# Performance work log

Hardware: AMD Instinct MI355X
Metric: run time of the kernel (lower is better)

Reference implementation:

```python
import jax, jax.numpy as jnp
import numpy as np
import math

B, S, D, H = 4, 2048, 1024, 16
DK = D // H  # 64


def setup_inputs() -> dict:
    key = jax.random.key(0)
    ks = jax.random.split(key, 8)
    sc = 1.0 / math.sqrt(D)
    Q = jax.random.normal(ks[0], (B, S, D), dtype=jnp.float32)
    K = jax.random.normal(ks[1], (B, S, D), dtype=jnp.float32)
    V = jax.random.normal(ks[2], (B, S, D), dtype=jnp.float32)
    # per-head projection weights, stacked: [H, D, DK]
    Wq = jax.random.normal(ks[3], (H, D, DK), dtype=jnp.float32) * sc
    Wk = jax.random.normal(ks[4], (H, D, DK), dtype=jnp.float32) * sc
    Wv = jax.random.normal(ks[5], (H, D, DK), dtype=jnp.float32) * sc
    Wo = jax.random.normal(ks[6], (D, D), dtype=jnp.float32) * sc
    bo = jax.random.normal(ks[7], (D,), dtype=jnp.float32) * sc
    mask = jnp.tril(jnp.ones((S, S), dtype=bool))  # causal
    return {"Q": Q, "K": K, "V": V, "mask": mask,
            "Wq": Wq, "Wk": Wk, "Wv": Wv, "Wo": Wo, "bo": bo}


def reference(Q, K, V, mask, Wq, Wk, Wv, Wo, bo):
    # batched per-head projections: [B,S,D] x [H,D,DK] -> [B,H,S,DK]
    q = jnp.einsum('bsd,hdk->bhsk', Q, Wq)
    k = jnp.einsum('bsd,hdk->bhsk', K, Wk)
    v = jnp.einsum('bsd,hdk->bhsk', V, Wv)
    # NOTE: source scales by k.shape[-1]/sqrt(d_k) = d_k/sqrt(d_k) = sqrt(d_k)
    scale = jnp.float32(DK / math.sqrt(DK))
    w = jnp.einsum('bhsk,bhtk->bhst', q, k) * scale  # [B,H,S,S]
    w = jnp.where(mask[None, None, :, :], w, jnp.float32(-jnp.inf))
    w = jax.nn.softmax(w, axis=-1)
    out = jnp.einsum('bhst,bhtk->bhsk', w, v)  # [B,H,S,DK]
    # concat heads along last dim (head order preserved): [B,S,D]
    concat = out.transpose(0, 2, 1, 3).reshape(B, S, D)
    # output projection (dropout p=0 -> identity in eval)
    return concat @ Wo.T + bo
```

## Files before the change

### kernel.cpp

```cpp
#include <hip/hip_runtime.h>
#include <math.h>


#define BB 4
#define SS 2048
#define DD 1024
#define HH 16
#define DKK 64
#define MM (BB * SS)

typedef unsigned short u16;
typedef _Float16 f16x8 __attribute__((ext_vector_type(8)));
typedef float f32x4 __attribute__((ext_vector_type(4)));
typedef __attribute__((address_space(1))) unsigned int gas_u32;
typedef __attribute__((address_space(3))) unsigned int las_u32;

__device__ __forceinline__ float bf2f(u16 u) {
    union { unsigned int i; float f; } c;
    c.i = ((unsigned int)u) << 16;
    return c.f;
}
__device__ __forceinline__ u16 f2h(float f) {
    _Float16 h = (_Float16)f;
    return __builtin_bit_cast(u16, h);
}
__device__ __forceinline__ void split1(float x, u16& hi, u16& lo) {
    _Float16 hh = (_Float16)x;
    hi = __builtin_bit_cast(u16, hh);
    lo = f2h(x - (float)hh);
}
__device__ __forceinline__ void gld16(const void* g, void* l) {
    __builtin_amdgcn_global_load_lds((gas_u32*)g, (las_u32*)l, 16, 0, 0);
}

__global__ void sniff_kernel(const u16* t0, const u16* t1, const u16* t2,
                             const u16* t3, const u16* t4, const u16* t5,
                             const u16* t6, const u16* t7, int* flags)
{
    const u16* ptrs[8] = {t0, t1, t2, t3, t4, t5, t6, t7};
    const u16* p = ptrs[blockIdx.x];
    int tid = threadIdx.x;
    int cnt = 0;
    #pragma unroll
    for (int i = 0; i < 8; i++) {
        u16 v = p[tid * 8 + i];
        int e = (v >> 7) & 0xFF;
        if (e >= 0xF0 || (e <= 0x0F && (v & 0x7FFF) != 0)) cnt++;
    }
    #pragma unroll
    for (int off = 32; off; off >>= 1) cnt += __shfl_down(cnt, off);
    if (tid == 0) flags[blockIdx.x] = (cnt >= 4) ? 1 : 0;
}

__global__ __launch_bounds__(256) void split_x_kernel(
    const void* __restrict__ X, const int* __restrict__ flags, int fidx,
    u16* __restrict__ Xh, u16* __restrict__ Xl)
{
    const int xf = flags[fidx];
    size_t idx = ((size_t)blockIdx.x * 256 + threadIdx.x) * 8;
    float x[8];
    if (xf) {
        float4 a = *(const float4*)((const float*)X + idx);
        float4 b = *(const float4*)((const float*)X + idx + 4);
        x[0] = a.x; x[1] = a.y; x[2] = a.z; x[3] = a.w;
        x[4] = b.x; x[5] = b.y; x[6] = b.z; x[7] = b.w;
    } else {
        ushort4 a = *(const ushort4*)((const u16*)X + idx);
        ushort4 b = *(const ushort4*)((const u16*)X + idx + 4);
        x[0] = bf2f(a.x); x[1] = bf2f(a.y); x[2] = bf2f(a.z); x[3] = bf2f(a.w);
        x[4] = bf2f(b.x); x[5] = bf2f(b.y); x[6] = bf2f(b.z); x[7] = bf2f(b.w);
    }
    union { u16 u[8]; uint4 v; } H, L;
    #pragma unroll
    for (int i = 0; i < 8; i++) split1(x[i], H.u[i], L.u[i]);
    *(uint4*)(Xh + idx) = H.v;
    *(uint4*)(Xl + idx) = L.v;
}

__global__ __launch_bounds__(256) void split_wqkv_kernel(
    const void* __restrict__ Wq, const void* __restrict__ Wk, const void* __restrict__ Wv,
    const int* __restrict__ flags, u16* __restrict__ Wth, u16* __restrict__ Wtl)
{
    const int z = blockIdx.z, h = blockIdx.y, kc = blockIdx.x;
    const void* __restrict__ W = (z == 0) ? Wq : (z == 1) ? Wk : Wv;
    const int wf = flags[3 + z];
    __shared__ float T[64][65];
    const int t = threadIdx.x;
    {
        const int kk = t >> 2, ns = (t & 3) * 16;
        const size_t base = (size_t)h * DD * DKK + (size_t)(kc * 64 + kk) * DKK + ns;
        #pragma unroll
        for (int j = 0; j < 4; j++) {
            if (wf) {
                float4 v = *(const float4*)((const float*)W + base + 4 * j);
                T[kk][ns + 4 * j + 0] = v.x; T[kk][ns + 4 * j + 1] = v.y;
                T[kk][ns + 4 * j + 2] = v.z; T[kk][ns + 4 * j + 3] = v.w;
            } else {
                ushort4 v = *(const ushort4*)((const u16*)W + base + 4 * j);
                T[kk][ns + 4 * j + 0] = bf2f(v.x); T[kk][ns + 4 * j + 1] = bf2f(v.y);
                T[kk][ns + 4 * j + 2] = bf2f(v.z); T[kk][ns + 4 * j + 3] = bf2f(v.w);
            }
        }
    }
    __syncthreads();
    {
        const int n = t >> 2, ks = (t & 3) * 16;
        union { u16 u[16]; uint4 v[2]; } Hv, Lv;
        #pragma unroll
        for (int i = 0; i < 16; i++) split1(T[ks + i][n], Hv.u[i], Lv.u[i]);
        size_t ob = ((size_t)(z * HH + h) * DKK + n) * DD + kc * 64 + ks;
        *(uint4*)(Wth + ob)     = Hv.v[0];
        *(uint4*)(Wth + ob + 8) = Hv.v[1];
        *(uint4*)(Wtl + ob)     = Lv.v[0];
        *(uint4*)(Wtl + ob + 8) = Lv.v[1];
    }
}

__global__ __launch_bounds__(256, 4) void proj_v3_kernel(
    const u16* __restrict__ Xh, const u16* __restrict__ Xl,
    const u16* __restrict__ Wth, const u16* __restrict__ Wtl,
    u16* __restrict__ out, int z)
{
    const int h0 = blockIdx.y * 2;
    const int m0 = blockIdx.x * 128;

    __shared__ __align__(16) u16 WH[128 * 64];
    __shared__ __align__(16) u16 WL[128 * 64];

    const int tid  = threadIdx.x;
    const int lane = tid & 63, wave = tid >> 6;
    const int quad = lane >> 4, ln = lane & 15;

    const int lr = lane >> 3, lg = (lane & 7) ^ (lane >> 3);
    const size_t wsrc0 = ((size_t)((z * HH + h0) * DKK) + wave * 32 + lr) * DD + lg * 8;
    const size_t arow = (size_t)(m0 + wave * 32 + ln) * DD + quad * 8;

    f32x4 acc[2][8];
    #pragma unroll
    for (int mh = 0; mh < 2; mh++)
        #pragma unroll
        for (int nt = 0; nt < 8; nt++)
            acc[mh][nt] = (f32x4){0.f, 0.f, 0.f, 0.f};

    for (int kbase = 0; kbase < DD; kbase += 64) {
        __syncthreads();
        f16x8 a_h[2][2], a_l[2][2];
        #pragma unroll
        for (int kh = 0; kh < 2; kh++)
            #pragma unroll
            for (int mh = 0; mh < 2; mh++) {
                size_t o = arow + (size_t)(mh * 16) * DD + kbase + kh * 32;
                a_h[kh][mh] = __builtin_bit_cast(f16x8, *(const uint4*)(Xh + o));
                a_l[kh][mh] = __builtin_bit_cast(f16x8, *(const uint4*)(Xl + o));
            }
        #pragma unroll
        for (int j = 0; j < 4; j++) {
            gld16(Wth + wsrc0 + (size_t)j * 8 * DD + kbase, &WH[(wave * 32 + j * 8) * 64]);
            gld16(Wtl + wsrc0 + (size_t)j * 8 * DD + kbase, &WL[(wave * 32 + j * 8) * 64]);
        }
        asm volatile("s_waitcnt vmcnt(0)" ::: "memory");
        __syncthreads();

        #pragma unroll
        for (int kh = 0; kh < 2; kh++) {
            const int kg = ((kh * 4 + quad) ^ (ln & 7)) * 8;
            #pragma unroll
            for (int nt = 0; nt < 8; nt++) {
                const int n = nt * 16 + ln;
                f16x8 bh = __builtin_bit_cast(f16x8, *(const uint4*)&WH[n * 64 + kg]);
                f16x8 bl = __builtin_bit_cast(f16x8, *(const uint4*)&WL[n * 64 + kg]);
                #pragma unroll
                for (int mh = 0; mh < 2; mh++) {
                    acc[mh][nt] = __builtin_amdgcn_mfma_f32_16x16x32_f16(a_l[kh][mh], bh, acc[mh][nt], 0, 0, 0);
                    acc[mh][nt] = __builtin_amdgcn_mfma_f32_16x16x32_f16(a_h[kh][mh], bl, acc[mh][nt], 0, 0, 0);
                    acc[mh][nt] = __builtin_amdgcn_mfma_f32_16x16x32_f16(a_h[kh][mh], bh, acc[mh][nt], 0, 0, 0);
                }
            }
        }
    }

    #pragma unroll
    for (int mh = 0; mh < 2; mh++)
        #pragma unroll
        for (int r = 0; r < 4; r++) {
            int m = m0 + wave * 32 + mh * 16 + quad * 4 + r;
            int b = m >> 11, s = m & 2047;
            #pragma unroll
            for (int nt = 0; nt < 8; nt++) {
                int head = h0 + (nt >> 2);
                u16* op = out + (((size_t)(b * HH + head) * SS + s)) * DKK;
                op[(nt & 3) * 16 + ln] = f2h(acc[mh][nt][r]);
            }
        }
}

__global__ __launch_bounds__(512) void attn_kernel(
    const u16* __restrict__ qb, const u16* __restrict__ kb,
    const u16* __restrict__ vb, u16* __restrict__ cath, u16* __restrict__ catl)
{
    __shared__ __align__(16) u16 Kt[64 * 72];
    __shared__ __align__(16) u16 Vt[64 * 72];
    __shared__ __align__(16) u16 Pw[8][16 * 72];

    const int tid  = threadIdx.x;
    const int lane = tid & 63, wave = tid >> 6;
    const int quad = lane >> 4, ln = lane & 15;

    const int p  = blockIdx.x;
    const int bh = (p >> 6) * 8 + (p & 7);
    const int pairidx = (p >> 3) & 7;
    const int b = bh >> 4, h = bh & 15;

    const int skey = tid >> 3, sseg = (tid & 7) * 8;
    const int vkey = tid & 63, vdkb = (tid >> 6) * 8;

    const u16* kbp = kb + (size_t)bh * SS * DKK;
    const u16* vbp = vb + (size_t)bh * SS * DKK;

    #pragma unroll 1
    for (int half = 0; half < 2; half++) {
        const int xt = half == 0 ? 15 - pairidx : pairidx;
        const int qbase = xt * 128;
        const int ktmax = 2 * xt + 1;

        const int wq = qbase + wave * 16;
        const int diagkt = wq >> 6;
        const int wqmax = wq + 15;

        const u16* qp = qb + ((size_t)bh * SS + wq + ln) * DKK;
        f16x8 qf0 = __builtin_bit_cast(f16x8, *(const uint4*)(qp + quad * 8));
        f16x8 qf1 = __builtin_bit_cast(f16x8, *(const uint4*)(qp + 32 + quad * 8));

        f32x4 acc[4];
        #pragma unroll
        for (int n = 0; n < 4; n++) acc[n] = (f32x4){0.f, 0.f, 0.f, 0.f};
        float mrow[4], lrow[4];
        #pragma unroll
        for (int r = 0; r < 4; r++) { mrow[r] = -INFINITY; lrow[r] = 0.f; }

        {
            uint4 ka = *(const uint4*)(kbp + (size_t)skey * DKK + sseg);
            uint4 va = *(const uint4*)(vbp + (size_t)vkey * DKK + vdkb);
            *(uint4*)&Kt[skey * 72 + sseg] = ka;
            u16 vv[8];
            *(uint4*)&vv[0] = va;
            #pragma unroll
            for (int i = 0; i < 8; i++)
                Vt[(vdkb + i) * 72 + vkey] = vv[i];
        }
        __syncthreads();

        for (int kt = 0; kt <= ktmax; ++kt) {
            uint4 ka, va;
            const bool pfb = (kt < ktmax);
            if (pfb) {
                ka = *(const uint4*)(kbp + (size_t)((kt + 1) * 64 + skey) * DKK + sseg);
                va = *(const uint4*)(vbp + (size_t)((kt + 1) * 64 + vkey) * DKK + vdkb);
            }

            if (kt * 64 <= wqmax) {
                f32x4 sa[4];
                #pragma unroll
                for (int n = 0; n < 4; n++) {
                    sa[n] = (f32x4){0.f, 0.f, 0.f, 0.f};
                    f16x8 kf0 = __builtin_bit_cast(f16x8,
                        *(const uint4*)&Kt[(n * 16 + ln) * 72 + quad * 8]);
                    sa[n] = __builtin_amdgcn_mfma_f32_16x16x32_f16(qf0, kf0, sa[n], 0, 0, 0);
                    f16x8 kf1 = __builtin_bit_cast(f16x8,
                        *(const uint4*)&Kt[(n * 16 + ln) * 72 + 32 + quad * 8]);
                    sa[n] = __builtin_amdgcn_mfma_f32_16x16x32_f16(qf1, kf1, sa[n], 0, 0, 0);
                }

                float sc[4][4];
                const bool diag = (kt == diagkt);
                #pragma unroll
                for (int n = 0; n < 4; n++)
                    #pragma unroll
                    for (int r = 0; r < 4; r++) {
                        float s = sa[n][r] * 8.0f;
                        if (diag && (kt * 64 + n * 16 + ln) > (wq + quad * 4 + r))
                            s = -INFINITY;
                        sc[n][r] = s;
                    }

                float rmax[4];
                #pragma unroll
                for (int r = 0; r < 4; r++)
                    rmax[r] = fmaxf(fmaxf(sc[0][r], sc[1][r]), fmaxf(sc[2][r], sc[3][r]));
                #pragma unroll
                for (int off = 1; off < 16; off <<= 1)
                    #pragma unroll
                    for (int r = 0; r < 4; r++)
                        rmax[r] = fmaxf(rmax[r], __shfl_xor(rmax[r], off));
                float alpha[4];
                #pragma unroll
                for (int r = 0; r < 4; r++) {
                    float mn = fmaxf(mrow[r], rmax[r]);
                    alpha[r] = __expf(mrow[r] - mn);
                    mrow[r] = mn;
                }
                u16* pw = Pw[wave];
                float lsum[4] = {0.f, 0.f, 0.f, 0.f};
                #pragma unroll
                for (int n = 0; n < 4; n++)
                    #pragma unroll
                    for (int r = 0; r < 4; r++) {
                        float pp = __expf(sc[n][r] - mrow[r]);
                        _Float16 ph = (_Float16)pp;
                        pw[(quad * 4 + r) * 72 + n * 16 + ln] = __builtin_bit_cast(u16, ph);
                        lsum[r] += (float)ph;
                    }
                #pragma unroll
                for (int off = 1; off < 16; off <<= 1)
                    #pragma unroll
                    for (int r = 0; r < 4; r++)
                        lsum[r] += __shfl_xor(lsum[r], off);
                #pragma unroll
                for (int r = 0; r < 4; r++)
                    lrow[r] = lrow[r] * alpha[r] + lsum[r];
                #pragma unroll
                for (int n = 0; n < 4; n++)
                    #pragma unroll
                    for (int r = 0; r < 4; r++)
                        acc[n][r] *= alpha[r];

                asm volatile("s_waitcnt lgkmcnt(0)" ::: "memory");
                f16x8 pf0 = __builtin_bit_cast(f16x8, *(const uint4*)&pw[ln * 72 + quad * 8]);
                f16x8 pf1 = __builtin_bit_cast(f16x8, *(const uint4*)&pw[ln * 72 + 32 + quad * 8]);

                #pragma unroll
                for (int n = 0; n < 4; n++) {
                    f16x8 vf0 = __builtin_bit_cast(f16x8,
                        *(const uint4*)&Vt[(n * 16 + ln) * 72 + quad * 8]);
                    acc[n] = __builtin_amdgcn_mfma_f32_16x16x32_f16(pf0, vf0, acc[n], 0, 0, 0);
                    f16x8 vf1 = __builtin_bit_cast(f16x8,
                        *(const uint4*)&Vt[(n * 16 + ln) * 72 + 32 + quad * 8]);
                    acc[n] = __builtin_amdgcn_mfma_f32_16x16x32_f16(pf1, vf1, acc[n], 0, 0, 0);
                }
            }

            __syncthreads();
            if (pfb) {
                *(uint4*)&Kt[skey * 72 + sseg] = ka;
                u16 vv[8];
                *(uint4*)&vv[0] = va;
                #pragma unroll
                for (int i = 0; i < 8; i++)
                    Vt[(vdkb + i) * 72 + vkey] = vv[i];
            }
            __syncthreads();
        }

        #pragma unroll
        for (int r = 0; r < 4; r++) {
            float inv = 1.0f / lrow[r];
            int row = wq + quad * 4 + r;
            size_t o = ((size_t)b * SS + row) * DD + h * DKK;
            #pragma unroll
            for (int n = 0; n < 4; n++) {
                float v = acc[n][r] * inv;
                u16 hh, ll;
                split1(v, hh, ll);
                cath[o + n * 16 + ln] = hh;
                catl[o + n * 16 + ln] = ll;
            }
        }
    }
}

__global__ __launch_bounds__(256, 4) void outproj_v3_kernel(
    const u16* __restrict__ Ah, const u16* __restrict__ Al,
    const u16* __restrict__ Woh, const u16* __restrict__ Wol,
    const void* __restrict__ bo, const int* __restrict__ flags,
    float* __restrict__ out)
{
    const int n0 = blockIdx.y * 128;
    const int m0 = blockIdx.x * 128;

    __shared__ __align__(16) u16 WH[128 * 64];
    __shared__ __align__(16) u16 WL[128 * 64];

    const int tid  = threadIdx.x;
    const int lane = tid & 63, wave = tid >> 6;
    const int quad = lane >> 4, ln = lane & 15;

    const int lr = lane >> 3, lg = (lane & 7) ^ (lane >> 3);
    const size_t wsrc0 = ((size_t)(n0 + wave * 32 + lr)) * DD + lg * 8;
    const size_t arow  = (size_t)(m0 + wave * 32 + ln) * DD + quad * 8;

    f32x4 acc[2][8];
    #pragma unroll
    for (int mh = 0; mh < 2; mh++)
        #pragma unroll
        for (int nt = 0; nt < 8; nt++)
            acc[mh][nt] = (f32x4){0.f, 0.f, 0.f, 0.f};

    for (int kbase = 0; kbase < DD; kbase += 64) {
        __syncthreads();
        f16x8 a_h[2][2], a_l[2][2];
        #pragma unroll
        for (int kh = 0; kh < 2; kh++)
            #pragma unroll
            for (int mh = 0; mh < 2; mh++) {
                size_t o = arow + (size_t)(mh * 16) * DD + kbase + kh * 32;
                a_h[kh][mh] = __builtin_bit_cast(f16x8, *(const uint4*)(Ah + o));
                a_l[kh][mh] = __builtin_bit_cast(f16x8, *(const uint4*)(Al + o));
            }
        #pragma unroll
        for (int j = 0; j < 4; j++) {
            gld16(Woh + wsrc0 + (size_t)j * 8 * DD + kbase, &WH[(wave * 32 + j * 8) * 64]);
            gld16(Wol + wsrc0 + (size_t)j * 8 * DD + kbase, &WL[(wave * 32 + j * 8) * 64]);
        }
        asm volatile("s_waitcnt vmcnt(0)" ::: "memory");
        __syncthreads();

        #pragma unroll
        for (int kh = 0; kh < 2; kh++) {
            const int kg = ((kh * 4 + quad) ^ (ln & 7)) * 8;
            #pragma unroll
            for (int nt = 0; nt < 8; nt++) {
                const int n = nt * 16 + ln;
                f16x8 bh = __builtin_bit_cast(f16x8, *(const uint4*)&WH[n * 64 + kg]);
                f16x8 bl = __builtin_bit_cast(f16x8, *(const uint4*)&WL[n * 64 + kg]);
                #pragma unroll
                for (int mh = 0; mh < 2; mh++) {
                    acc[mh][nt] = __builtin_amdgcn_mfma_f32_16x16x32_f16(a_l[kh][mh], bh, acc[mh][nt], 0, 0, 0);
                    acc[mh][nt] = __builtin_amdgcn_mfma_f32_16x16x32_f16(a_h[kh][mh], bl, acc[mh][nt], 0, 0, 0);
                    acc[mh][nt] = __builtin_amdgcn_mfma_f32_16x16x32_f16(a_h[kh][mh], bh, acc[mh][nt], 0, 0, 0);
                }
            }
        }
    }

    const int bf = flags[7];
    float bias[8];
    #pragma unroll
    for (int nt = 0; nt < 8; nt++) {
        int n = n0 + nt * 16 + ln;
        bias[nt] = bf ? ((const float*)bo)[n] : bf2f(((const u16*)bo)[n]);
    }
    #pragma unroll
    for (int mh = 0; mh < 2; mh++)
        #pragma unroll
        for (int r = 0; r < 4; r++) {
            int m = m0 + wave * 32 + mh * 16 + quad * 4 + r;
            float* op = out + (size_t)m * DD + n0;
            #pragma unroll
            for (int nt = 0; nt < 8; nt++)
                op[nt * 16 + ln] = acc[mh][nt][r] + bias[nt];
        }
}

extern "C" void kernel_launch(void* const* d_in, const int* in_sizes, int n_in,
                              void* d_out, int out_size, void* d_ws, size_t ws_size,
                              hipStream_t stream)
{
    const void* Q = d_in[0];
    const void* K = d_in[1];
    const void* V = d_in[2];
    const int widx = (n_in >= 9) ? 4 : 3;
    const void* Wq = d_in[widx + 0];
    const void* Wk = d_in[widx + 1];
    const void* Wv = d_in[widx + 2];
    const void* Wo = d_in[widx + 3];
    const void* bo = d_in[widx + 4];
    float* out = (float*)d_out;

    const size_t per = (size_t)BB * HH * SS * DKK;
    u16* qb = (u16*)d_ws;
    u16* kb = qb + per;
    u16* vb = kb + per;
    u16* xc = vb + per;
    u16* Xh = xc;
    u16* Xl = xc + per;
    u16* cath = xc;
    u16* catl = xc + per;
    const size_t wtn = (size_t)3 * HH * DKK * DD;
    u16* Wth = xc + 2 * per;
    u16* Wtl = Wth + wtn;
    u16* Woh = Wtl + wtn;
    u16* Wol = Woh + (size_t)DD * DD;
    int* flags = (int*)(Wol + (size_t)DD * DD);

    sniff_kernel<<<8, 64, 0, stream>>>(
        (const u16*)Q, (const u16*)K, (const u16*)V,
        (const u16*)Wq, (const u16*)Wk, (const u16*)Wv,
        (const u16*)Wo, (const u16*)bo, flags);

    split_wqkv_kernel<<<dim3(DD / 64, HH, 3), 256, 0, stream>>>(
        Wq, Wk, Wv, flags, Wth, Wtl);
    split_x_kernel<<<(DD * DD) / 2048, 256, 0, stream>>>(Wo, flags, 6, Woh, Wol);

    dim3 gp(MM / 128, HH / 2);
    split_x_kernel<<<(MM * DD) / 2048, 256, 0, stream>>>(Q, flags, 0, Xh, Xl);
    proj_v3_kernel<<<gp, 256, 0, stream>>>(Xh, Xl, Wth, Wtl, qb, 0);
    split_x_kernel<<<(MM * DD) / 2048, 256, 0, stream>>>(K, flags, 1, Xh, Xl);
    proj_v3_kernel<<<gp, 256, 0, stream>>>(Xh, Xl, Wth, Wtl, kb, 1);
    split_x_kernel<<<(MM * DD) / 2048, 256, 0, stream>>>(V, flags, 2, Xh, Xl);
    proj_v3_kernel<<<gp, 256, 0, stream>>>(Xh, Xl, Wth, Wtl, vb, 2);

    attn_kernel<<<(SS / 256) * BB * HH, 512, 0, stream>>>(qb, kb, vb, cath, catl);

    outproj_v3_kernel<<<dim3(MM / 128, DD / 128), 256, 0, stream>>>(
        cath, catl, Woh, Wol, bo, flags, out);
}
```

Baseline: 490.0 us.

## Fuse input split into QKV projection and double-buffer swizzled attention tiles

Removes the three split_x passes by reading the raw Q/K/V inputs directly inside the projection kernel and splitting them into high/low f16 on the fly. The three projection launches merge into one grid indexed by blockIdx.z. The attention kernel switches from padded LDS tiles to XOR-swizzled 64-wide tiles, double-buffers K/V, and drops one barrier per key tile. The cost is extra conversion ALU work on the A operand, repeated once per head-pair block instead of once per input. It also raises attention LDS use, which may lower occupancy.

Measured after the change: 470.6 us. 1.04x faster.

```diff
diff --git a/kernel.cpp b/kernel.cpp
--- a/kernel.cpp
+++ b/kernel.cpp
@@ -116,11 +116,16 @@
     }
 }
 
-__global__ __launch_bounds__(256, 4) void proj_v3_kernel(
-    const u16* __restrict__ Xh, const u16* __restrict__ Xl,
+__global__ __launch_bounds__(256, 4) void proj_v4_kernel(
+    const void* __restrict__ Q, const void* __restrict__ K, const void* __restrict__ V,
     const u16* __restrict__ Wth, const u16* __restrict__ Wtl,
-    u16* __restrict__ out, int z)
-{
+    const int* __restrict__ flags,
+    u16* __restrict__ qb, u16* __restrict__ kb, u16* __restrict__ vb)
+{
+    const int z = blockIdx.z;
+    const void* __restrict__ X = (z == 0) ? Q : (z == 1) ? K : V;
+    u16* __restrict__ out      = (z == 0) ? qb : (z == 1) ? kb : vb;
+    const int xf = flags[z];
     const int h0 = blockIdx.y * 2;
     const int m0 = blockIdx.x * 128;
 
@@ -150,8 +155,23 @@
             #pragma unroll
             for (int mh = 0; mh < 2; mh++) {
                 size_t o = arow + (size_t)(mh * 16) * DD + kbase + kh * 32;
-                a_h[kh][mh] = __builtin_bit_cast(f16x8, *(const uint4*)(Xh + o));
-                a_l[kh][mh] = __builtin_bit_cast(f16x8, *(const uint4*)(Xl + o));
+                float x[8];
+                if (xf) {
+                    float4 a = *(const float4*)((const float*)X + o);
+                    float4 b = *(const float4*)((const float*)X + o + 4);
+                    x[0] = a.x; x[1] = a.y; x[2] = a.z; x[3] = a.w;
+                    x[4] = b.x; x[5] = b.y; x[6] = b.z; x[7] = b.w;
+                } else {
+                    ushort4 a = *(const ushort4*)((const u16*)X + o);
+                    ushort4 b = *(const ushort4*)((const u16*)X + o + 4);
+                    x[0] = bf2f(a.x); x[1] = bf2f(a.y); x[2] = bf2f(a.z); x[3] = bf2f(a.w);
+                    x[4] = bf2f(b.x); x[5] = bf2f(b.y); x[6] = bf2f(b.z); x[7] = bf2f(b.w);
+                }
+                union { u16 u[8]; f16x8 v; } H, L;
+                #pragma unroll
+                for (int i = 0; i < 8; i++) split1(x[i], H.u[i], L.u[i]);
+                a_h[kh][mh] = H.v;
+                a_l[kh][mh] = L.v;
             }
         #pragma unroll
         for (int j = 0; j < 4; j++) {
@@ -198,9 +218,9 @@
     const u16* __restrict__ qb, const u16* __restrict__ kb,
     const u16* __restrict__ vb, u16* __restrict__ cath, u16* __restrict__ catl)
 {
-    __shared__ __align__(16) u16 Kt[64 * 72];
-    __shared__ __align__(16) u16 Vt[64 * 72];
-    __shared__ __align__(16) u16 Pw[8][16 * 72];
+    __shared__ __align__(16) u16 Kt[2][64 * 64];
+    __shared__ __align__(16) u16 Vt[2][64 * 64];
+    __shared__ __align__(16) u16 Pw[8][16 * 64];
 
     const int tid  = threadIdx.x;
     const int lane = tid & 63, wave = tid >> 6;
@@ -211,7 +231,8 @@
     const int pairidx = (p >> 3) & 7;
     const int b = bh >> 4, h = bh & 15;
 
-    const int skey = tid >> 3, sseg = (tid & 7) * 8;
+    const int skey = tid >> 3, kgrp = tid & 7;
+    const int koff = skey * 64 + ((kgrp ^ (skey & 7)) << 3);
     const int vkey = tid & 63, vdkb = (tid >> 6) * 8;
 
     const u16* kbp = kb + (size_t)bh * SS * DKK;
@@ -239,35 +260,41 @@
         for (int r = 0; r < 4; r++) { mrow[r] = -INFINITY; lrow[r] = 0.f; }
 
         {
-            uint4 ka = *(const uint4*)(kbp + (size_t)skey * DKK + sseg);
+            uint4 ka = *(const uint4*)(kbp + (size_t)skey * DKK + kgrp * 8);
             uint4 va = *(const uint4*)(vbp + (size_t)vkey * DKK + vdkb);
-            *(uint4*)&Kt[skey * 72 + sseg] = ka;
+            *(uint4*)&Kt[0][koff] = ka;
             u16 vv[8];
             *(uint4*)&vv[0] = va;
             #pragma unroll
-            for (int i = 0; i < 8; i++)
-                Vt[(vdkb + i) * 72 + vkey] = vv[i];
+            for (int i = 0; i < 8; i++) {
+                int row = vdkb + i;
+                Vt[0][row * 64 + (((vkey >> 3) ^ (row & 7)) << 3) + (vkey & 7)] = vv[i];
+            }
         }
         __syncthreads();
 
+        int cur = 0;
         for (int kt = 0; kt <= ktmax; ++kt) {
             uint4 ka, va;
             const bool pfb = (kt < ktmax);
             if (pfb) {
-                ka = *(const uint4*)(kbp + (size_t)((kt + 1) * 64 + skey) * DKK + sseg);
+                ka = *(const uint4*)(kbp + (size_t)((kt + 1) * 64 + skey) * DKK + kgrp * 8);
                 va = *(const uint4*)(vbp + (size_t)((kt + 1) * 64 + vkey) * DKK + vdkb);
             }
 
             if (kt * 64 <= wqmax) {
+                const u16* KT = Kt[cur];
+                const u16* VT = Vt[cur];
                 f32x4 sa[4];
                 #pragma unroll
                 for (int n = 0; n < 4; n++) {
                     sa[n] = (f32x4){0.f, 0.f, 0.f, 0.f};
+                    const int krow = n * 16 + ln;
                     f16x8 kf0 = __builtin_bit_cast(f16x8,
-                        *(const uint4*)&Kt[(n * 16 + ln) * 72 + quad * 8]);
+                        *(const uint4*)&KT[krow * 64 + ((quad ^ (ln & 7)) << 3)]);
                     sa[n] = __builtin_amdgcn_mfma_f32_16x16x32_f16(qf0, kf0, sa[n], 0, 0, 0);
                     f16x8 kf1 = __builtin_bit_cast(f16x8,
-                        *(const uint4*)&Kt[(n * 16 + ln) * 72 + 32 + quad * 8]);
+                        *(const uint4*)&KT[krow * 64 + (((quad + 4) ^ (ln & 7)) << 3)]);
                     sa[n] = __builtin_amdgcn_mfma_f32_16x16x32_f16(qf1, kf1, sa[n], 0, 0, 0);
                 }
 
@@ -307,7 +334,9 @@
                     for (int r = 0; r < 4; r++) {
                         float pp = __expf(sc[n][r] - mrow[r]);
                         _Float16 ph = (_Float16)pp;
-                        pw[(quad * 4 + r) * 72 + n * 16 + ln] = __builtin_bit_cast(u16, ph);
+                        const int row = quad * 4 + r;
+                        pw[row * 64 + (((n * 2 + (ln >> 3)) ^ (row & 7)) << 3) + (ln & 7)]
+                            = __builtin_bit_cast(u16, ph);
                         lsum[r] += (float)ph;
                     }
                 #pragma unroll
@@ -325,30 +354,35 @@
                         acc[n][r] *= alpha[r];
 
                 asm volatile("s_waitcnt lgkmcnt(0)" ::: "memory");
-                f16x8 pf0 = __builtin_bit_cast(f16x8, *(const uint4*)&pw[ln * 72 + quad * 8]);
-                f16x8 pf1 = __builtin_bit_cast(f16x8, *(const uint4*)&pw[ln * 72 + 32 + quad * 8]);
+                f16x8 pf0 = __builtin_bit_cast(f16x8,
+                    *(const uint4*)&pw[ln * 64 + ((quad ^ (ln & 7)) << 3)]);
+                f16x8 pf1 = __builtin_bit_cast(f16x8,
+                    *(const uint4*)&pw[ln * 64 + (((quad + 4) ^ (ln & 7)) << 3)]);
 
                 #pragma unroll
                 for (int n = 0; n < 4; n++) {
+                    const int vrow = n * 16 + ln;
                     f16x8 vf0 = __builtin_bit_cast(f16x8,
-                        *(const uint4*)&Vt[(n * 16 + ln) * 72 + quad * 8]);
+                        *(const uint4*)&VT[vrow * 64 + ((quad ^ (ln & 7)) << 3)]);
                     acc[n] = __builtin_amdgcn_mfma_f32_16x16x32_f16(pf0, vf0, acc[n], 0, 0, 0);
                     f16x8 vf1 = __builtin_bit_cast(f16x8,
-                        *(const uint4*)&Vt[(n * 16 + ln) * 72 + 32 + quad * 8]);
+                        *(const uint4*)&VT[vrow * 64 + (((quad + 4) ^ (ln & 7)) << 3)]);
                     acc[n] = __builtin_amdgcn_mfma_f32_16x16x32_f16(pf1, vf1, acc[n], 0, 0, 0);
                 }
             }
 
-            __syncthreads();
             if (pfb) {
-                *(uint4*)&Kt[skey * 72 + sseg] = ka;
+                *(uint4*)&Kt[cur ^ 1][koff] = ka;
                 u16 vv[8];
                 *(uint4*)&vv[0] = va;
                 #pragma unroll
-                for (int i = 0; i < 8; i++)
-                    Vt[(vdkb + i) * 72 + vkey] = vv[i];
+                for (int i = 0; i < 8; i++) {
+                    int row = vdkb + i;
+                    Vt[cur ^ 1][row * 64 + (((vkey >> 3) ^ (row & 7)) << 3) + (vkey & 7)] = vv[i];
+                }
             }
             __syncthreads();
+            cur ^= 1;
         }
 
         #pragma unroll
@@ -470,13 +504,10 @@
     u16* qb = (u16*)d_ws;
     u16* kb = qb + per;
     u16* vb = kb + per;
-    u16* xc = vb + per;
-    u16* Xh = xc;
-    u16* Xl = xc + per;
-    u16* cath = xc;
-    u16* catl = xc + per;
+    u16* cath = vb + per;
+    u16* catl = cath + per;
     const size_t wtn = (size_t)3 * HH * DKK * DD;
-    u16* Wth = xc + 2 * per;
+    u16* Wth = catl + per;
     u16* Wtl = Wth + wtn;
     u16* Woh = Wtl + wtn;
     u16* Wol = Woh + (size_t)DD * DD;
@@ -491,13 +522,8 @@
         Wq, Wk, Wv, flags, Wth, Wtl);
     split_x_kernel<<<(DD * DD) / 2048, 256, 0, stream>>>(Wo, flags, 6, Woh, Wol);
 
-    dim3 gp(MM / 128, HH / 2);
-    split_x_kernel<<<(MM * DD) / 2048, 256, 0, stream>>>(Q, flags, 0, Xh, Xl);
-    proj_v3_kernel<<<gp, 256, 0, stream>>>(Xh, Xl, Wth, Wtl, qb, 0);
-    split_x_kernel<<<(MM * DD) / 2048, 256, 0, stream>>>(K, flags, 1, Xh, Xl);
-    proj_v3_kernel<<<gp, 256, 0, stream>>>(Xh, Xl, Wth, Wtl, kb, 1);
-    split_x_kernel<<<(MM * DD) / 2048, 256, 0, stream>>>(V, flags, 2, Xh, Xl);
-    proj_v3_kernel<<<gp, 256, 0, stream>>>(Xh, Xl, Wth, Wtl, vb, 2);
+    proj_v4_kernel<<<dim3(MM / 128, HH / 2, 3), 256, 0, stream>>>(
+        Q, K, V, Wth, Wtl, flags, qb, kb, vb);
 
     attn_kernel<<<(SS / 256) * BB * HH, 512, 0, stream>>>(qb, kb, vb, cath, catl);
 
```
